# Kernel optimization log

Hardware: AMD Instinct MI355X
Metric: run time of the kernel (lower is better)

The kernel has to match this reference:

```python
import jax, jax.numpy as jnp
import numpy as np

B, S, D = 256, 1024, 32   # batch, seq_len, raw feature dim
H, L = 128, 2             # hidden_dim, num_layers
IN = D + 2                # GRU input: features + mask + time-delta


def setup_inputs() -> dict:
    key = jax.random.key(0)
    ks = jax.random.split(key, 16)
    x = jax.random.normal(ks[0], (B, S, D), jnp.float32)
    nan_mask = jax.random.bernoulli(ks[1], 0.3, (B, S))
    x = jnp.where(nan_mask[:, :, None], jnp.nan, x)  # missing timesteps are all-NaN
    # strictly increasing timestamps shared across batch
    t = jnp.cumsum(jax.random.uniform(ks[2], (S,), jnp.float32, 0.1, 1.0))

    def init(k, shape):
        s = 1.0 / np.sqrt(H)
        return jax.random.uniform(k, shape, jnp.float32, -s, s)

    params = {}
    in_dims = [IN, H]
    for l in range(L):
        params[f"Wih{l}"] = init(ks[3 + 4 * l], (3 * H, in_dims[l]))
        params[f"Whh{l}"] = init(ks[4 + 4 * l], (3 * H, H))
        params[f"bih{l}"] = init(ks[5 + 4 * l], (3 * H,))
        params[f"bhh{l}"] = init(ks[6 + 4 * l], (3 * H,))
    return {"t": t, "x": x, **params}


def _impute(t, x):
    # mask[b,i] = 1 if timestep i of sample b is missing (any NaN feature)
    mask = jnp.isnan(x).any(-1)                      # [B,S] bool
    # prev[b,i] = last observed index strictly before i, or -1 (parallel cummax)
    idx = jnp.where(~mask, jnp.arange(S)[None, :], -1)
    cmax = jax.lax.cummax(idx, axis=1)
    prev = jnp.concatenate([jnp.full((B, 1), -1), cmax[:, :-1]], axis=1)  # [B,S]
    prev_c = jnp.clip(prev, 0, S - 1)
    x_clean = jnp.nan_to_num(x)
    x_prev = jnp.take_along_axis(x_clean, prev_c[:, :, None], axis=1)
    # masked: forward-fill from last observation (zeros if none); unmasked: keep x
    imputed = jnp.where(mask[:, :, None],
                        jnp.where((prev >= 0)[:, :, None], x_prev, 0.0),
                        x_clean)
    # time delta: t[i]-t[prev] when a previous observation exists, else raw t delta
    t_deltas = jnp.concatenate([jnp.zeros((1,), t.dtype), t[1:] - t[:-1]])
    t_exp = jnp.where(prev >= 0, t[None, :] - t[prev_c], t_deltas[None, :])  # [B,S]
    return jnp.concatenate([imputed,
                            mask.astype(jnp.float32)[:, :, None],
                            t_exp[:, :, None]], axis=-1)  # [B,S,D+2]


def _gru_layer(xseq, Wih, Whh, bih, bhh):
    # precompute input projections for all timesteps (one big GEMM)
    gx = jnp.einsum('bsd,gd->bsg', xseq, Wih) + bih  # [B,S,3H], gate order r,z,n

    def step(h, g):
        gh = h @ Whh.T + bhh
        r = jax.nn.sigmoid(g[:, :H] + gh[:, :H])
        z = jax.nn.sigmoid(g[:, H:2 * H] + gh[:, H:2 * H])
        n = jnp.tanh(g[:, 2 * H:] + r * gh[:, 2 * H:])
        h = (1.0 - z) * n + z * h
        return h, h

    h0 = jnp.zeros((xseq.shape[0], H), xseq.dtype)
    _, hs = jax.lax.scan(step, h0, gx.transpose(1, 0, 2))
    return hs.transpose(1, 0, 2)  # [B,S,H]


def reference(t, x, Wih0, Whh0, bih0, bhh0, Wih1, Whh1, bih1, bhh1):
    inp = _impute(t, x)
    h = _gru_layer(inp, Wih0, Whh0, bih0, bhh0)
    h = _gru_layer(h, Wih1, Whh1, bih1, bhh1)
    return h[:, -1, :]  # [B,H]
```

## Files before the change

kernel.cpp:

```cpp
#include <hip/hip_runtime.h>
#include <hip/hip_bf16.h>


#define BB 256
#define SS 1024
#define DD 32
#define HH 128
#define NT 512

typedef _Float16 f16;
typedef __attribute__((ext_vector_type(2))) _Float16 h2;

__device__ inline h2 as_h2(int x) { union { int i; h2 h; } u; u.i = x; return u.h; }

__device__ inline float dot2(h2 a, h2 b, float c) {
    return __builtin_amdgcn_fdot2(a, b, c, false);
}

__device__ inline float frcp(float x) { return __builtin_amdgcn_rcpf(x); }
__device__ inline float fast_sigm(float x) { return frcp(1.0f + __expf(-x)); }
__device__ inline float fast_tanh(float x) {
    x = fminf(15.0f, fmaxf(-15.0f, x));
    float e = __expf(-2.0f * x);
    return (1.0f - e) * frcp(1.0f + e);
}

struct ImpState { float xprev, tprev; bool hasprev; };

__device__ inline void impute_store(int i, float xv, int l, ImpState& st,
                                    f16* hxf, const float* tb) {
    bool nanp = (l < 32) && (xv != xv);
    unsigned long long bal = __ballot(nanp);
    bool mask = bal != 0ull;
    if (l < 32) {
        float imp = mask ? st.xprev : xv;
        hxf[l] = (f16)imp;
        if (!mask) st.xprev = xv;
    }
    float tcur = tb[i];
    float tdel = (i == 0) ? 0.0f : (tcur - tb[i - 1]);
    float texp = st.hasprev ? (tcur - st.tprev) : tdel;
    if (l == 32) hxf[32] = (f16)(mask ? 1.0f : 0.0f);
    if (l == 33) hxf[33] = (f16)texp;
    if (!mask) { st.hasprev = true; st.tprev = tcur; }
}

__global__ __launch_bounds__(NT, 2) void gru_fused(
    const float* __restrict__ t_in, const float* __restrict__ x_in,
    const float* __restrict__ Wih0, const float* __restrict__ Whh0,
    const float* __restrict__ bih0, const float* __restrict__ bhh0,
    const float* __restrict__ Wih1, const float* __restrict__ Whh1,
    const float* __restrict__ bih1, const float* __restrict__ bhh1,
    float* __restrict__ out)
{
    __shared__ float tb[SS];
    __shared__ int stDW[145];
    __shared__ float pGX0[384], pGH0[384], pGX1[384], pGH1[384];

    const int tid = threadIdx.x;
    const int lane = tid & 63;
    const int b = blockIdx.x;
    const bool isDot = (tid < 384);

    h2 w[192];
    if (isDot) {
        const float* pa = Whh0 + tid * HH;
        const float* pb = Wih1 + tid * HH;
        const float* pc = Wih0 + tid * 34;
        #pragma unroll
        for (int k = 0; k < 64; k++) { h2 v = {(f16)pa[2*k], (f16)pa[2*k+1]}; w[k] = v; }
        #pragma unroll
        for (int k = 0; k < 64; k++) { h2 v = {(f16)pb[2*k], (f16)pb[2*k+1]}; w[64+k] = v; }
        #pragma unroll
        for (int k = 0; k < 17; k++) { h2 v = {(f16)pc[2*k], (f16)pc[2*k+1]}; w[128+k] = v; }
        #pragma unroll
        for (int k = 145; k < 192; k++) { h2 v = {(f16)0.0f, (f16)0.0f}; w[k] = v; }
    } else {
        const int gl = tid - 384;
        const float* p0 = Whh1 + (size_t)gl * HH;
        const float* p1 = Whh1 + (size_t)(gl + 128) * HH;
        const float* p2 = Whh1 + (size_t)(gl + 256) * HH;
        #pragma unroll
        for (int k = 0; k < 64; k++) { h2 v = {(f16)p0[2*k], (f16)p0[2*k+1]}; w[k] = v; }
        #pragma unroll
        for (int k = 0; k < 64; k++) { h2 v = {(f16)p1[2*k], (f16)p1[2*k+1]}; w[64+k] = v; }
        #pragma unroll
        for (int k = 0; k < 64; k++) { h2 v = {(f16)p2[2*k], (f16)p2[2*k+1]}; w[128+k] = v; }
    }

    float hra = 0.0f, hrb = 0.0f;
    float bra = 0, bza = 0, bina = 0, bhna = 0, brb = 0, bzb = 0, binb = 0, bhnb = 0;
    if (!isDot) {
        const bool u0 = (tid < 448);
        const float* bi = u0 ? bih0 : bih1;
        const float* bh = u0 ? bhh0 : bhh1;
        const int ua = 2 * lane, ub = ua + 1;
        bra = bi[ua] + bh[ua];       bza = bi[ua+128] + bh[ua+128];
        bina = bi[ua+256];           bhna = bh[ua+256];
        brb = bi[ub] + bh[ub];       bzb = bi[ub+128] + bh[ub+128];
        binb = bi[ub+256];           bhnb = bh[ub+256];
    }

    for (int i2 = tid; i2 < SS; i2 += NT) tb[i2] = t_in[i2];
    if (tid < 128) stDW[tid] = 0;
    f16* hxf = (f16*)&stDW[128];

    const float* xrow = x_in + (size_t)b * SS * DD + tid;
    ImpState st; st.xprev = 0.0f; st.tprev = 0.0f; st.hasprev = false;

    __syncthreads();
    if (tid < 64) {
        float xv0 = (tid < 32) ? xrow[0] : 0.0f;
        impute_store(0, xv0, tid, st, hxf, tb);
    }
    __syncthreads();

    const int idxA = isDot ? lane : (64 + lane);
    const int idxB = 128 + ((lane < 17) ? lane : 0);

    for (int i = 0; i <= SS; ++i) {
        const bool doL0 = (i < SS), doL1 = (i > 0), doImp = (i + 1 < SS);

        int vA = stDW[idxA];

        float xv_n = 0.0f;
        if (tid < 32 && doImp) xv_n = xrow[(size_t)(i + 1) * DD];

        if (isDot) {
            int vB = stDW[idxB];
            float aGH0 = 0.0f, aGX1 = 0.0f, aGX0 = 0.0f;
            #pragma unroll
            for (int k = 0; k < 64; k++) {
                h2 s = as_h2(__builtin_amdgcn_readlane(vA, k));
                aGH0 = dot2(s, w[k],      aGH0);
                aGX1 = dot2(s, w[64 + k], aGX1);
            }
            #pragma unroll
            for (int k = 0; k < 17; k++) {
                h2 s = as_h2(__builtin_amdgcn_readlane(vB, k));
                aGX0 = dot2(s, w[128 + k], aGX0);
            }
            pGH0[tid] = aGH0; pGX1[tid] = aGX1; pGX0[tid] = aGX0;
        } else {
            const int gl = tid - 384;
            float a0 = 0.0f, a1 = 0.0f, a2 = 0.0f;
            #pragma unroll
            for (int k = 0; k < 64; k++) {
                h2 s = as_h2(__builtin_amdgcn_readlane(vA, k));
                a0 = dot2(s, w[k],       a0);
                a1 = dot2(s, w[64 + k],  a1);
                a2 = dot2(s, w[128 + k], a2);
            }
            pGH1[gl] = a0; pGH1[gl + 128] = a1; pGH1[gl + 256] = a2;
        }
        __syncthreads();

        if (!isDot) {
            const bool u0 = (tid < 448);
            if (u0 ? doL0 : doL1) {
                const float* gx = u0 ? pGX0 : pGX1;
                const float* gh = u0 ? pGH0 : pGH1;
                const int ua = 2 * lane, ub = ua + 1;
                float r0 = fast_sigm(bra + gx[ua] + gh[ua]);
                float z0 = fast_sigm(bza + gx[ua+128] + gh[ua+128]);
                float n0 = fast_tanh(bina + gx[ua+256] + r0 * (bhna + gh[ua+256]));
                hra = (1.0f - z0) * n0 + z0 * hra;
                float r1 = fast_sigm(brb + gx[ub] + gh[ub]);
                float z1 = fast_sigm(bzb + gx[ub+128] + gh[ub+128]);
                float n1 = fast_tanh(binb + gx[ub+256] + r1 * (bhnb + gh[ub+256]));
                hrb = (1.0f - z1) * n1 + z1 * hrb;
                h2 hv = {(f16)hra, (f16)hrb};
                ((h2*)stDW)[(u0 ? 0 : 64) + lane] = hv;
            }
        } else if (tid < 64 && doImp) {
            impute_store(i + 1, xv_n, tid, st, hxf, tb);
        }
        __syncthreads();
    }

    if (tid >= 448) {
        float2 o = make_float2(hra, hrb);
        *(float2*)&out[(size_t)b * HH + 2 * lane] = o;
    }
}

extern "C" void kernel_launch(void* const* d_in, const int* in_sizes, int n_in,
                              void* d_out, int out_size, void* d_ws, size_t ws_size,
                              hipStream_t stream) {
    gru_fused<<<dim3(BB), dim3(NT), 0, stream>>>(
        (const float*)d_in[0], (const float*)d_in[1],
        (const float*)d_in[2], (const float*)d_in[3],
        (const float*)d_in[4], (const float*)d_in[5],
        (const float*)d_in[6], (const float*)d_in[7],
        (const float*)d_in[8], (const float*)d_in[9],
        (float*)d_out);
}
```

Before: 1.548 ms.

## Replace per-thread dot2 GRU recurrence with MFMA 16x16x32 matrix ops

Rewrites the fused two-layer GRU step so each of 8 waves owns 16 hidden units and computes gate pre-activations with MFMA f16 instructions, instead of readlane-broadcast fdot2 loops. Hidden states are double-buffered in shared memory, which removes the second barrier per timestep and the shared gate staging arrays. Gate nonlinearities are fused into the same waves that produce the MFMA accumulators. The cost is that each MFMA uses a broadcast B operand where only one column is useful, wasting most of its throughput, and weight fragments take many registers.

```diff
diff --git a/kernel.cpp b/kernel.cpp
--- a/kernel.cpp
+++ b/kernel.cpp
@@ -10,12 +10,14 @@
 
 typedef _Float16 f16;
 typedef __attribute__((ext_vector_type(2))) _Float16 h2;
-
+typedef __attribute__((ext_vector_type(8))) _Float16 h8;
+typedef __attribute__((ext_vector_type(4))) float fx4;
+
+__device__ inline fx4 mfma(h8 a, h8 b, fx4 c) {
+    return __builtin_amdgcn_mfma_f32_16x16x32_f16(a, b, c, 0, 0, 0);
+}
 __device__ inline h2 as_h2(int x) { union { int i; h2 h; } u; u.i = x; return u.h; }
-
-__device__ inline float dot2(h2 a, h2 b, float c) {
-    return __builtin_amdgcn_fdot2(a, b, c, false);
-}
+__device__ inline int h2_int(h2 h) { union { h2 h; int i; } u; u.h = h; return u.i; }
 
 __device__ inline float frcp(float x) { return __builtin_amdgcn_rcpf(x); }
 __device__ inline float fast_sigm(float x) { return frcp(1.0f + __expf(-x)); }
@@ -27,21 +29,23 @@
 
 struct ImpState { float xprev, tprev; bool hasprev; };
 
-__device__ inline void impute_store(int i, float xv, int l, ImpState& st,
-                                    f16* hxf, const float* tb) {
-    bool nanp = (l < 32) && (xv != xv);
+__device__ inline void impute_store(int i, float xv, int lane, ImpState& st,
+                                    f16* hxd, int* scld, const float* tb) {
+    bool nanp = (lane < 32) && (xv != xv);
     unsigned long long bal = __ballot(nanp);
     bool mask = bal != 0ull;
-    if (l < 32) {
+    if (lane < 32) {
         float imp = mask ? st.xprev : xv;
-        hxf[l] = (f16)imp;
+        hxd[lane] = (f16)imp;
         if (!mask) st.xprev = xv;
     }
     float tcur = tb[i];
     float tdel = (i == 0) ? 0.0f : (tcur - tb[i - 1]);
     float texp = st.hasprev ? (tcur - st.tprev) : tdel;
-    if (l == 32) hxf[32] = (f16)(mask ? 1.0f : 0.0f);
-    if (l == 33) hxf[33] = (f16)texp;
+    if (lane == 0) {
+        h2 s; s.x = (f16)(mask ? 1.0f : 0.0f); s.y = (f16)texp;
+        *scld = h2_int(s);
+    }
     if (!mask) { st.hasprev = true; st.tprev = tcur; }
 }
 
@@ -54,133 +58,169 @@
     float* __restrict__ out)
 {
     __shared__ float tb[SS];
-    __shared__ int stDW[145];
-    __shared__ float pGX0[384], pGH0[384], pGX1[384], pGH1[384];
+    __shared__ alignas(16) f16 h0s[2][HH];
+    __shared__ alignas(16) f16 h1s[2][HH];
+    __shared__ alignas(16) f16 hxs[2][32];
+    __shared__ int scl[2];
 
     const int tid = threadIdx.x;
     const int lane = tid & 63;
+    const int w = tid >> 6;
+    const int q = lane >> 4;
+    const int m = lane & 15;
     const int b = blockIdx.x;
-    const bool isDot = (tid < 384);
-
-    h2 w[192];
-    if (isDot) {
-        const float* pa = Whh0 + tid * HH;
-        const float* pb = Wih1 + tid * HH;
-        const float* pc = Wih0 + tid * 34;
+
+    h8 whh0f[3][4], wih1f[3][4], whh1f[3][4], wih0c0[3];
+    h2 wih0c1[3];
+    #pragma unroll
+    for (int g = 0; g < 3; g++) {
+        const int row = 128 * g + 16 * w + m;
+        const float* pa = Whh0 + (size_t)row * HH;
+        const float* pb = Wih1 + (size_t)row * HH;
+        const float* pc = Whh1 + (size_t)row * HH;
+        const float* pd = Wih0 + (size_t)row * 34;
         #pragma unroll
-        for (int k = 0; k < 64; k++) { h2 v = {(f16)pa[2*k], (f16)pa[2*k+1]}; w[k] = v; }
+        for (int c = 0; c < 4; c++) {
+            h8 va, vb, vc;
+            #pragma unroll
+            for (int j = 0; j < 8; j++) {
+                int k = 32 * c + 8 * q + j;
+                va[j] = (f16)pa[k]; vb[j] = (f16)pb[k]; vc[j] = (f16)pc[k];
+            }
+            whh0f[g][c] = va; wih1f[g][c] = vb; whh1f[g][c] = vc;
+        }
+        h8 vd;
         #pragma unroll
-        for (int k = 0; k < 64; k++) { h2 v = {(f16)pb[2*k], (f16)pb[2*k+1]}; w[64+k] = v; }
+        for (int j = 0; j < 8; j++) vd[j] = (f16)pd[8 * q + j];
+        wih0c0[g] = vd;
+        h2 t; t.x = (f16)pd[32]; t.y = (f16)pd[33]; wih0c1[g] = t;
+    }
+
+    fx4 bR0, bZ0, bNi0, bNh0, bR1, bZ1, bNi1, bNh1;
+    #pragma unroll
+    for (int e = 0; e < 4; e++) {
+        int r4 = 16 * w + 4 * q + e;
+        bR0[e]  = bih0[r4] + bhh0[r4];
+        bZ0[e]  = bih0[128 + r4] + bhh0[128 + r4];
+        bNi0[e] = bih0[256 + r4];
+        bNh0[e] = bhh0[256 + r4];
+        bR1[e]  = bih1[r4] + bhh1[r4];
+        bZ1[e]  = bih1[128 + r4] + bhh1[128 + r4];
+        bNi1[e] = bih1[256 + r4];
+        bNh1[e] = bhh1[256 + r4];
+    }
+
+    for (int i2 = tid; i2 < SS; i2 += NT) tb[i2] = t_in[i2];
+    if (tid < 128)      ((int*)h0s)[tid] = 0;
+    else if (tid < 256) ((int*)h1s)[tid - 128] = 0;
+
+    const float* xrow = x_in + (size_t)b * SS * DD + lane;
+    ImpState st; st.xprev = 0.0f; st.tprev = 0.0f; st.hasprev = false;
+    fx4 hn0 = {0.f, 0.f, 0.f, 0.f}, hn1 = {0.f, 0.f, 0.f, 0.f};
+
+    __syncthreads();
+    if (w == 0) {
+        float xv0 = (lane < 32) ? xrow[0] : 0.0f;
+        impute_store(0, xv0, lane, st, hxs[0], &scl[0], tb);
+    }
+    __syncthreads();
+
+    for (int i = 0; i <= SS; ++i) {
+        const int p = i & 1, np = p ^ 1;
+        const bool doL0 = (i < SS), doL1 = (i > 0), doImp = (i + 1 < SS);
+
+        float xnext = 0.0f;
+        if (w == 0 && lane < 32 && doImp) xnext = xrow[(size_t)(i + 1) * DD];
+
+        const f16* h0p = h0s[p];
+        h8 b0[4];
         #pragma unroll
-        for (int k = 0; k < 17; k++) { h2 v = {(f16)pc[2*k], (f16)pc[2*k+1]}; w[128+k] = v; }
-        #pragma unroll
-        for (int k = 145; k < 192; k++) { h2 v = {(f16)0.0f, (f16)0.0f}; w[k] = v; }
-    } else {
-        const int gl = tid - 384;
-        const float* p0 = Whh1 + (size_t)gl * HH;
-        const float* p1 = Whh1 + (size_t)(gl + 128) * HH;
-        const float* p2 = Whh1 + (size_t)(gl + 256) * HH;
-        #pragma unroll
-        for (int k = 0; k < 64; k++) { h2 v = {(f16)p0[2*k], (f16)p0[2*k+1]}; w[k] = v; }
-        #pragma unroll
-        for (int k = 0; k < 64; k++) { h2 v = {(f16)p1[2*k], (f16)p1[2*k+1]}; w[64+k] = v; }
-        #pragma unroll
-        for (int k = 0; k < 64; k++) { h2 v = {(f16)p2[2*k], (f16)p2[2*k+1]}; w[128+k] = v; }
-    }
-
-    float hra = 0.0f, hrb = 0.0f;
-    float bra = 0, bza = 0, bina = 0, bhna = 0, brb = 0, bzb = 0, binb = 0, bhnb = 0;
-    if (!isDot) {
-        const bool u0 = (tid < 448);
-        const float* bi = u0 ? bih0 : bih1;
-        const float* bh = u0 ? bhh0 : bhh1;
-        const int ua = 2 * lane, ub = ua + 1;
-        bra = bi[ua] + bh[ua];       bza = bi[ua+128] + bh[ua+128];
-        bina = bi[ua+256];           bhna = bh[ua+256];
-        brb = bi[ub] + bh[ub];       bzb = bi[ub+128] + bh[ub+128];
-        binb = bi[ub+256];           bhnb = bh[ub+256];
-    }
-
-    for (int i2 = tid; i2 < SS; i2 += NT) tb[i2] = t_in[i2];
-    if (tid < 128) stDW[tid] = 0;
-    f16* hxf = (f16*)&stDW[128];
-
-    const float* xrow = x_in + (size_t)b * SS * DD + tid;
-    ImpState st; st.xprev = 0.0f; st.tprev = 0.0f; st.hasprev = false;
-
-    __syncthreads();
-    if (tid < 64) {
-        float xv0 = (tid < 32) ? xrow[0] : 0.0f;
-        impute_store(0, xv0, tid, st, hxf, tb);
-    }
-    __syncthreads();
-
-    const int idxA = isDot ? lane : (64 + lane);
-    const int idxB = 128 + ((lane < 17) ? lane : 0);
-
-    for (int i = 0; i <= SS; ++i) {
-        const bool doL0 = (i < SS), doL1 = (i > 0), doImp = (i + 1 < SS);
-
-        int vA = stDW[idxA];
-
-        float xv_n = 0.0f;
-        if (tid < 32 && doImp) xv_n = xrow[(size_t)(i + 1) * DD];
-
-        if (isDot) {
-            int vB = stDW[idxB];
-            float aGH0 = 0.0f, aGX1 = 0.0f, aGX0 = 0.0f;
-            #pragma unroll
-            for (int k = 0; k < 64; k++) {
-                h2 s = as_h2(__builtin_amdgcn_readlane(vA, k));
-                aGH0 = dot2(s, w[k],      aGH0);
-                aGX1 = dot2(s, w[64 + k], aGX1);
-            }
-            #pragma unroll
-            for (int k = 0; k < 17; k++) {
-                h2 s = as_h2(__builtin_amdgcn_readlane(vB, k));
-                aGX0 = dot2(s, w[128 + k], aGX0);
-            }
-            pGH0[tid] = aGH0; pGX1[tid] = aGX1; pGX0[tid] = aGX0;
-        } else {
-            const int gl = tid - 384;
-            float a0 = 0.0f, a1 = 0.0f, a2 = 0.0f;
-            #pragma unroll
-            for (int k = 0; k < 64; k++) {
-                h2 s = as_h2(__builtin_amdgcn_readlane(vA, k));
-                a0 = dot2(s, w[k],       a0);
-                a1 = dot2(s, w[64 + k],  a1);
-                a2 = dot2(s, w[128 + k], a2);
-            }
-            pGH1[gl] = a0; pGH1[gl + 128] = a1; pGH1[gl + 256] = a2;
+        for (int c = 0; c < 4; c++) b0[c] = *(const h8*)(h0p + 32 * c + 8 * q);
+
+        if (doL0) {
+            h8 bx0 = *(const h8*)(hxs[p] + 8 * q);
+            h2 scv = as_h2(scl[p]);
+            h8 bx1;
+            #pragma unroll
+            for (int j = 0; j < 8; j++) bx1[j] = (f16)0.0f;
+            bx1[0] = (q == 0) ? scv.x : (f16)0.0f;
+            bx1[1] = (q == 0) ? scv.y : (f16)0.0f;
+            fx4 r = bR0, z = bZ0, ni = bNi0, nh = bNh0;
+            r  = mfma(wih0c0[0], bx0, r);
+            z  = mfma(wih0c0[1], bx0, z);
+            ni = mfma(wih0c0[2], bx0, ni);
+            #pragma unroll
+            for (int g = 0; g < 3; g++) {
+                h8 a1;
+                #pragma unroll
+                for (int j = 0; j < 8; j++) a1[j] = (f16)0.0f;
+                a1[0] = wih0c1[g].x; a1[1] = wih0c1[g].y;
+                if (g == 0) r = mfma(a1, bx1, r);
+                else if (g == 1) z = mfma(a1, bx1, z);
+                else ni = mfma(a1, bx1, ni);
+            }
+            #pragma unroll
+            for (int c = 0; c < 4; c++) {
+                r  = mfma(whh0f[0][c], b0[c], r);
+                z  = mfma(whh0f[1][c], b0[c], z);
+                nh = mfma(whh0f[2][c], b0[c], nh);
+            }
+            #pragma unroll
+            for (int e = 0; e < 4; e++) {
+                float rr = fast_sigm(r[e]);
+                float zz = fast_sigm(z[e]);
+                float nn = fast_tanh(ni[e] + rr * nh[e]);
+                hn0[e] = (1.0f - zz) * nn + zz * hn0[e];
+            }
+            if (m == 0) {
+                h2 lo; lo.x = (f16)hn0[0]; lo.y = (f16)hn0[1];
+                h2 hi; hi.x = (f16)hn0[2]; hi.y = (f16)hn0[3];
+                h2* dst = (h2*)(h0s[np] + 16 * w + 4 * q);
+                dst[0] = lo; dst[1] = hi;
+            }
         }
+
+        if (doL1) {
+            fx4 r1 = bR1, z1 = bZ1, ni1 = bNi1, nh1 = bNh1;
+            #pragma unroll
+            for (int c = 0; c < 4; c++) {
+                r1  = mfma(wih1f[0][c], b0[c], r1);
+                z1  = mfma(wih1f[1][c], b0[c], z1);
+                ni1 = mfma(wih1f[2][c], b0[c], ni1);
+            }
+            const f16* h1p = h1s[p];
+            h8 b1[4];
+            #pragma unroll
+            for (int c = 0; c < 4; c++) b1[c] = *(const h8*)(h1p + 32 * c + 8 * q);
+            #pragma unroll
+            for (int c = 0; c < 4; c++) {
+                r1  = mfma(whh1f[0][c], b1[c], r1);
+                z1  = mfma(whh1f[1][c], b1[c], z1);
+                nh1 = mfma(whh1f[2][c], b1[c], nh1);
+            }
+            #pragma unroll
+            for (int e = 0; e < 4; e++) {
+                float rr = fast_sigm(r1[e]);
+                float zz = fast_sigm(z1[e]);
+                float nn = fast_tanh(ni1[e] + rr * nh1[e]);
+                hn1[e] = (1.0f - zz) * nn + zz * hn1[e];
+            }
+            if (m == 0) {
+                h2 lo; lo.x = (f16)hn1[0]; lo.y = (f16)hn1[1];
+                h2 hi; hi.x = (f16)hn1[2]; hi.y = (f16)hn1[3];
+                h2* dst = (h2*)(h1s[np] + 16 * w + 4 * q);
+                dst[0] = lo; dst[1] = hi;
+            }
+        }
+
+        if (w == 0 && doImp)
+            impute_store(i + 1, xnext, lane, st, hxs[np], &scl[np], tb);
+
         __syncthreads();
-
-        if (!isDot) {
-            const bool u0 = (tid < 448);
-            if (u0 ? doL0 : doL1) {
-                const float* gx = u0 ? pGX0 : pGX1;
-                const float* gh = u0 ? pGH0 : pGH1;
-                const int ua = 2 * lane, ub = ua + 1;
-                float r0 = fast_sigm(bra + gx[ua] + gh[ua]);
-                float z0 = fast_sigm(bza + gx[ua+128] + gh[ua+128]);
-                float n0 = fast_tanh(bina + gx[ua+256] + r0 * (bhna + gh[ua+256]));
-                hra = (1.0f - z0) * n0 + z0 * hra;
-                float r1 = fast_sigm(brb + gx[ub] + gh[ub]);
-                float z1 = fast_sigm(bzb + gx[ub+128] + gh[ub+128]);
-                float n1 = fast_tanh(binb + gx[ub+256] + r1 * (bhnb + gh[ub+256]));
-                hrb = (1.0f - z1) * n1 + z1 * hrb;
-                h2 hv = {(f16)hra, (f16)hrb};
-                ((h2*)stDW)[(u0 ? 0 : 64) + lane] = hv;
-            }
-        } else if (tid < 64 && doImp) {
-            impute_store(i + 1, xv_n, tid, st, hxf, tb);
-        }
-        __syncthreads();
-    }
-
-    if (tid >= 448) {
-        float2 o = make_float2(hra, hrb);
-        *(float2*)&out[(size_t)b * HH + 2 * lane] = o;
+    }
+
+    if (m == 0) {
+        *(fx4*)(out + (size_t)b * HH + 16 * w + 4 * q) = hn1;
     }
 }
 
```

New measurement: 1.597 ms. 1.03x slower.
